# Optimization experiments

Measured on AMD Instinct MI355X. Metric: run time of the kernel, lower is better.

Reference implementation:

```python
import jax, jax.numpy as jnp
import numpy as np

B, CIN, BINS, FRAMES = 8, 2, 1024, 512
NQ = 4
C = 2 * NQ          # number of quantizer channels
E = 1024            # codebook size
BETA = 0.25         # commitment cost


def conv2d(x, w, b, pad):
    y = jax.lax.conv_general_dilated(
        x, w, window_strides=(1, 1),
        padding=((pad[0], pad[0]), (pad[1], pad[1])),
        dimension_numbers=("NCHW", "OIHW", "NCHW"))
    return y + b[None, :, None, None]


def setup_inputs() -> dict:
    key = jax.random.key(0)
    ks = jax.random.split(key, 6)
    return {
        "x": jax.random.normal(ks[0], (B, CIN, BINS, FRAMES), jnp.float32),
        "conv1_w": jax.random.normal(ks[1], (C, CIN, 9, 1), jnp.float32) * 0.1,
        "conv1_b": jnp.zeros((C,), jnp.float32),
        "conv2_w": jax.random.normal(ks[2], (C, C, 9, 1), jnp.float32) * 0.05,
        "conv2_b": jnp.zeros((C,), jnp.float32),
        "skip_w": jax.random.normal(ks[3], (C, CIN, 1, 1), jnp.float32) * 0.1,
        "skip_b": jnp.zeros((C,), jnp.float32),
        "codebooks": jax.random.normal(ks[4], (C, E, BINS), jnp.float32),
    }


def reference(x, conv1_w, conv1_b, conv2_w, conv2_b, skip_w, skip_b, codebooks):
    # ResBlock projection: 2 -> 2*num_quantizers channels, (9,1) convs along bins
    h = conv2d(x, conv1_w, conv1_b, (4, 0))
    h = jax.nn.leaky_relu(h, 0.2)
    h = conv2d(h, conv2_w, conv2_b, (4, 0))
    h = h + conv2d(x, skip_w, skip_b, (0, 0))          # [B, C, BINS, F]

    # Batched VQ across all C quantizers at once.
    # Per-frame vectors: [C, N, BINS] with N = B*FRAMES
    v = jnp.transpose(h, (1, 0, 3, 2)).reshape(C, B * FRAMES, BINS)
    x2 = jnp.sum(v * v, axis=-1, keepdims=True)                     # [C,N,1]
    e2 = jnp.sum(codebooks * codebooks, axis=-1)[:, None, :]        # [C,1,E]
    d = x2 + e2 - 2.0 * jnp.einsum("cnb,ceb->cne", v, codebooks)    # [C,N,E]
    idx = jnp.argmin(d, axis=-1)                                    # [C,N]
    q = jax.vmap(lambda cb, i: cb[i])(codebooks, idx)               # [C,N,BINS]

    # VQ-VAE loss (codebook + commitment), summed over the 2Q quantizers
    sg = jax.lax.stop_gradient
    cb_loss = jnp.mean((q - sg(v)) ** 2, axis=(1, 2))
    cm_loss = jnp.mean((sg(q) - v) ** 2, axis=(1, 2))
    loss = jnp.sum(cb_loss + BETA * cm_loss)

    # straight-through estimator
    q_st = v + sg(q - v)                                            # [C,N,BINS]
    q_st = q_st.reshape(C, B, FRAMES, BINS).transpose(1, 0, 3, 2)   # [B,C,BINS,F]
    # torch loop prepends each new q: final channel order is reversed
    embedded = q_st[:, ::-1]
    return embedded, loss
```

## Files before the change

### kernel.cpp

```cpp
#include <hip/hip_runtime.h>

namespace {

constexpr int kB = 8, kCin = 2, kBins = 1024, kFrames = 512;
constexpr int kC = 8, kE = 1024, kN = kB * kFrames;

typedef _Float16 f16x8 __attribute__((ext_vector_type(8)));
typedef float f32x4 __attribute__((ext_vector_type(4)));

union HPack4 { _Float16 h[4]; uint2 u; };
union HPack2 { _Float16 h[2]; unsigned int u; };

__device__ inline void splitf(float v, _Float16& h, _Float16& l) {
    float a = (fabsf(v) >= 6.103515625e-05f) ? v : 0.f;
    _Float16 hh = (_Float16)a;
    h = hh;
    l = (_Float16)((v - (float)hh) * 4096.0f);
}

constexpr int BT = 32, FT = 32, XB = BT + 16, HB = BT + 8;

__global__ __launch_bounds__(512, 4) void conv_fused_v2d(
    const float* __restrict__ x,
    const float* __restrict__ w1, const float* __restrict__ b1,
    const float* __restrict__ w2, const float* __restrict__ b2,
    const float* __restrict__ wsk, const float* __restrict__ bsk,
    _Float16* __restrict__ V1, float* __restrict__ partials)
{
    __shared__ float xt[kCin][XB][33];
    __shared__ float h1t[kC][HB][33];
    __shared__ float vbuf[2][BT][33];
    __shared__ float w1s[kC * kCin * 9];
    __shared__ float w2s[kC * kC][12];
    __shared__ float wsks[kC * kCin];
    __shared__ float b1s[kC], b2s[kC], bsks[kC];
    __shared__ float reds[8];

    const int t = threadIdx.x;
    const int bt = blockIdx.x, ft = blockIdx.y, bb = blockIdx.z;
    const int bs = bt * BT, f0 = ft * FT;
    _Float16* V2 = V1 + (size_t)33554432;

    if (t < kC * kCin * 9) w1s[t] = w1[t];
    for (int i = t; i < 768; i += 512) {
        int cc = i / 12, k = i % 12;
        w2s[cc][k] = (k < 9) ? w2[cc * 9 + k] : 0.f;
    }
    if (t < kC * kCin) wsks[t] = wsk[t];
    if (t < kC) { b1s[t] = b1[t]; b2s[t] = b2[t]; bsks[t] = bsk[t]; }

    for (int i = t; i < kCin * XB * FT; i += 512) {
        int fi = i % FT, xb = (i / FT) % XB, ci = i / (FT * XB);
        int gb = bs - 8 + xb;
        float v = 0.f;
        if (gb >= 0 && gb < kBins)
            v = x[((bb * kCin + ci) * kBins + gb) * kFrames + f0 + fi];
        xt[ci][xb][fi] = v;
    }
    __syncthreads();

    const int fi = t & 31;
    const int r = t >> 5;
    const int cm = r & 7, rh = r >> 3;

    #pragma unroll
    for (int qi = 0; qi < 3; qi++) {
        const int q = qi * 2 + rh;
        if (q < 5) {
            float a8[8];
            #pragma unroll
            for (int jj = 0; jj < 8; jj++) a8[jj] = b1s[cm];
            #pragma unroll
            for (int ci = 0; ci < kCin; ci++) {
                float w[16];
                #pragma unroll
                for (int k = 0; k < 16; k++) w[k] = xt[ci][q * 8 + k][fi];
                const float* wp = &w1s[(cm * kCin + ci) * 9];
                #pragma unroll
                for (int jj = 0; jj < 8; jj++)
                    #pragma unroll
                    for (int k = 0; k < 9; k++)
                        a8[jj] += w[jj + k] * wp[k];
            }
            #pragma unroll
            for (int jj = 0; jj < 8; jj++) {
                int hb = q * 8 + jj;
                int gb = bs - 4 + hb;
                float v = (gb >= 0 && gb < kBins) ? (a8[jj] > 0.f ? a8[jj] : 0.2f * a8[jj]) : 0.f;
                h1t[cm][hb][fi] = v;
            }
        }
    }
    __syncthreads();

    float acc[8][2];
    #pragma unroll
    for (int c = 0; c < 8; c++)
        #pragma unroll
        for (int j = 0; j < 2; j++) acc[c][j] = b2s[c] + bsks[c];

    for (int ci = 0; ci < 8; ci++) {
        float w[10];
        #pragma unroll
        for (int k = 0; k < 10; k++) w[k] = h1t[ci][r * 2 + k][fi];
        #pragma unroll
        for (int c = 0; c < 8; c++) {
            const float4* wp4 = (const float4*)&w2s[c * 8 + ci][0];
            float4 wA = wp4[0], wB = wp4[1], wC = wp4[2];
            float wk[9] = {wA.x, wA.y, wA.z, wA.w, wB.x, wB.y, wB.z, wB.w, wC.x};
            #pragma unroll
            for (int j = 0; j < 2; j++) {
                float s = 0.f;
                #pragma unroll
                for (int k = 0; k < 9; k++) s += w[j + k] * wk[k];
                acc[c][j] += s;
            }
        }
    }
    #pragma unroll
    for (int j = 0; j < 2; j++) {
        float x0 = xt[0][r * 2 + j + 8][fi];
        float x1 = xt[1][r * 2 + j + 8][fi];
        #pragma unroll
        for (int c = 0; c < 8; c++)
            acc[c][j] += x0 * wsks[c * 2] + x1 * wsks[c * 2 + 1];
    }

    float sq = 0.f;
    #pragma unroll
    for (int c = 0; c < 8; c++)
        #pragma unroll
        for (int j = 0; j < 2; j++) sq += acc[c][j] * acc[c][j];

    const int rn = t >> 4, kq = t & 15;
    #pragma unroll 1
    for (int c = 0; c < 8; c++) {
        vbuf[c & 1][fi][r * 2 + 0] = acc[c][0];
        vbuf[c & 1][fi][r * 2 + 1] = acc[c][1];
        __syncthreads();
        float v0 = vbuf[c & 1][rn][kq * 2 + 0];
        float v1 = vbuf[c & 1][rn][kq * 2 + 1];
        HPack2 ph, pl;
        splitf(v0, ph.h[0], pl.h[0]);
        splitf(v1, ph.h[1], pl.h[1]);
        const int ng = bb * kFrames + f0 + rn;
        const size_t off = ((size_t)(c * kN + ng)) * kBins + bs + kq * 2;
        *(unsigned int*)&V1[off] = ph.u;
        *(unsigned int*)&V2[off] = pl.u;
    }

    #pragma unroll
    for (int off = 32; off > 0; off >>= 1) sq += __shfl_down(sq, off);
    if ((t & 63) == 0) reds[t >> 6] = sq;
    __syncthreads();
    if (t == 0) {
        float s = 0.f;
        #pragma unroll
        for (int i = 0; i < 8; i++) s += reds[i];
        int blin = (bb * gridDim.y + blockIdx.y) * gridDim.x + blockIdx.x;
        partials[blin] = s;
    }
}

__global__ __launch_bounds__(256) void cbsplit_e2(
    const float* __restrict__ cb, _Float16* __restrict__ B1,
    float* __restrict__ e2, unsigned long long* __restrict__ pk)
{
    const int gid = blockIdx.x * 256 + threadIdx.x;
    if (gid < kC * kN) pk[gid] = ~0ull;

    const int gw = gid >> 6;
    const int lane = threadIdx.x & 63;
    _Float16* B2 = B1 + (size_t)8388608;
    const float* row = cb + (size_t)gw * kBins;
    float s = 0.f;
    #pragma unroll
    for (int j = 0; j < 4; j++) {
        float4 v = *(const float4*)&row[lane * 4 + j * 256];
        s += v.x * v.x + v.y * v.y + v.z * v.z + v.w * v.w;
        HPack4 ph, pl;
        splitf(v.x, ph.h[0], pl.h[0]);
        splitf(v.y, ph.h[1], pl.h[1]);
        splitf(v.z, ph.h[2], pl.h[2]);
        splitf(v.w, ph.h[3], pl.h[3]);
        size_t off = (size_t)gw * kBins + lane * 4 + j * 256;
        *(uint2*)&B1[off] = ph.u;
        *(uint2*)&B2[off] = pl.u;
    }
    #pragma unroll
    for (int off = 32; off > 0; off >>= 1) s += __shfl_down(s, off);
    if (lane == 0) e2[gw] = s;
}

__global__ __launch_bounds__(512, 2) void dist_mfma(
    const _Float16* __restrict__ V1, const _Float16* __restrict__ B1p,
    const float* __restrict__ e2, unsigned long long* __restrict__ pk)
{
    __shared__ char smem[3 * 49152 + 2048];

    const int t = threadIdx.x;
    const int bidx = blockIdx.x;
    const int ch = bidx & 7;
    const int eh = (bidx >> 3) & 1;
    const int n0 = (bidx >> 4) * 256;
    const int w = t >> 6, lane = t & 63;
    const int l15 = lane & 15, kc4 = lane >> 4;
    const int wm = w >> 1, we = w & 1;

    float* lds_e2 = (float*)(smem + 147456);
    lds_e2[t] = e2[ch * kE + eh * 512 + t];

    const _Float16* srcA[4];
    int dstA[4];
    #pragma unroll
    for (int i = 0; i < 4; i++) {
        int ci = i * 512 + t;
        int row = ci >> 3, slot = ci & 7;
        int g = slot ^ (row & 7);
        int p = g >> 2, kc = g & 3;
        srcA[i] = V1 + (size_t)p * 33554432 + ((size_t)(ch * kN + n0 + row)) * kBins + kc * 8;
        dstA[i] = ci * 16;
    }
    const _Float16* srcB[2];
    int dstB[2];
    #pragma unroll
    for (int i = 0; i < 2; i++) {
        int bi = i * 512 + t;
        int row = bi >> 3, slot = bi & 7;
        int g = slot ^ (row & 7);
        int p = g >> 2, kc = g & 3;
        srcB[i] = B1p + (size_t)p * 8388608 + ((size_t)(ch * kE + row)) * kBins + kc * 8;
        dstB[i] = 32768 + bi * 16;
    }

    const int rowA = wm * 64 + l15;
    const int rowB = we * 64 + l15;
    const int baseA1 = rowA * 128 + ((kc4) ^ (rowA & 7)) * 16;
    const int baseA2 = rowA * 128 + ((4 + kc4) ^ (rowA & 7)) * 16;
    const int baseB1 = 32768 + rowB * 128 + ((kc4) ^ (rowB & 7)) * 16;
    const int baseB2 = 32768 + rowB * 128 + ((4 + kc4) ^ (rowB & 7)) * 16;

    float rm[16];
    int ri[16];
    #pragma unroll
    for (int s = 0; s < 16; s++) { rm[s] = 3.4e38f; ri[s] = 0; }

    typedef const __attribute__((address_space(1))) void gsrc_t;
    typedef __attribute__((address_space(3))) void gdst_t;

    auto issue = [&](int jj, int bw) {
        const int k0 = (jj & 31) * 32;
        const size_t etoff = (size_t)(eh * 4 + (jj >> 5)) * 128 * kBins + k0;
        char* nb = smem + bw * 49152;
        #pragma unroll
        for (int i = 0; i < 4; i++)
            __builtin_amdgcn_global_load_lds((gsrc_t*)(srcA[i] + k0), (gdst_t*)(nb + dstA[i]), 16, 0, 0);
        #pragma unroll
        for (int i = 0; i < 2; i++)
            __builtin_amdgcn_global_load_lds((gsrc_t*)(srcB[i] + etoff), (gdst_t*)(nb + dstB[i]), 16, 0, 0);
    };

    __syncthreads();

    issue(0, 0);
    issue(1, 1);
    int bread = 0, bwrite = 2;

    #pragma unroll 1
    for (int et = 0; et < 4; et++) {
        f32x4 hi[4][4], lo[4][4];
        #pragma unroll
        for (int mi = 0; mi < 4; mi++)
            #pragma unroll
            for (int ei = 0; ei < 4; ei++) {
                hi[mi][ei] = (f32x4){0.f, 0.f, 0.f, 0.f};
                lo[mi][ei] = (f32x4){0.f, 0.f, 0.f, 0.f};
            }

        #pragma unroll 1
        for (int ks = 0; ks < 32; ks++) {
            const int j = et * 32 + ks;
            if (j < 127)
                asm volatile("s_waitcnt vmcnt(6)\n\ts_barrier" ::: "memory");
            else
                asm volatile("s_waitcnt vmcnt(0)\n\ts_barrier" ::: "memory");
            if (j < 126) {
                issue(j + 2, bwrite);
                bwrite = (bwrite == 2) ? 0 : bwrite + 1;
            }

            const char* buf = smem + bread * 49152;
            bread = (bread == 2) ? 0 : bread + 1;

            f16x8 a1[4], a2[4], b1f[4], b2f[4];
            #pragma unroll
            for (int mi = 0; mi < 4; mi++) {
                a1[mi] = *(const f16x8*)(buf + baseA1 + mi * 2048);
                a2[mi] = *(const f16x8*)(buf + baseA2 + mi * 2048);
            }
            #pragma unroll
            for (int ei = 0; ei < 4; ei++) {
                b1f[ei] = *(const f16x8*)(buf + baseB1 + ei * 2048);
                b2f[ei] = *(const f16x8*)(buf + baseB2 + ei * 2048);
            }
            __builtin_amdgcn_s_setprio(1);
            #pragma unroll
            for (int mi = 0; mi < 4; mi++)
                #pragma unroll
                for (int ei = 0; ei < 4; ei++) {
                    hi[mi][ei] = __builtin_amdgcn_mfma_f32_16x16x32_f16(a1[mi], b1f[ei], hi[mi][ei], 0, 0, 0);
                    lo[mi][ei] = __builtin_amdgcn_mfma_f32_16x16x32_f16(a1[mi], b2f[ei], lo[mi][ei], 0, 0, 0);
                    lo[mi][ei] = __builtin_amdgcn_mfma_f32_16x16x32_f16(a2[mi], b1f[ei], lo[mi][ei], 0, 0, 0);
                }
            __builtin_amdgcn_s_setprio(0);
        }

        #pragma unroll
        for (int ei = 0; ei < 4; ei++) {
            const int eloc = et * 128 + we * 64 + ei * 16 + l15;
            const float ev = lds_e2[eloc];
            const int eix = eh * 512 + eloc;
            #pragma unroll
            for (int mi = 0; mi < 4; mi++) {
                f32x4 dot4 = hi[mi][ei] + lo[mi][ei] * (1.0f / 4096.0f);
                #pragma unroll
                for (int rr = 0; rr < 4; rr++) {
                    float d = ev - 2.0f * dot4[rr];
                    int s = mi * 4 + rr;
                    if (d < rm[s]) { rm[s] = d; ri[s] = eix; }
                }
            }
        }
    }

    #pragma unroll
    for (int m = 1; m < 16; m <<= 1) {
        #pragma unroll
        for (int s = 0; s < 16; s++) {
            float ov = __shfl_xor(rm[s], m);
            int oi = __shfl_xor(ri[s], m);
            if (ov < rm[s] || (ov == rm[s] && oi < ri[s])) { rm[s] = ov; ri[s] = oi; }
        }
    }

    float* mv = (float*)smem;
    int* miv = (int*)(smem + 2048);
    __syncthreads();
    if (l15 == 0) {
        #pragma unroll
        for (int s = 0; s < 16; s++) {
            int mi = s >> 2, rr = s & 3;
            int rloc = wm * 64 + mi * 16 + (lane >> 4) * 4 + rr;
            mv[rloc * 2 + we] = rm[s];
            miv[rloc * 2 + we] = ri[s];
        }
    }
    __syncthreads();
    if (t < 256) {
        float v0 = mv[t * 2], v1 = mv[t * 2 + 1];
        int i0 = miv[t * 2], i1 = miv[t * 2 + 1];
        bool take1 = (v1 < v0) || (v1 == v0 && i1 < i0);
        float bv = take1 ? v1 : v0;
        int bi = take1 ? i1 : i0;
        unsigned int u = __float_as_uint(bv);
        unsigned int su = (u & 0x80000000u) ? ~u : (u ^ 0x80000000u);
        unsigned long long packed = ((unsigned long long)su << 32) | (unsigned int)bi;
        atomicMin(&pk[ch * kN + n0 + t], packed);
    }
}

__global__ __launch_bounds__(256) void gather_pk(
    const float* __restrict__ cb, const unsigned long long* __restrict__ pk,
    const float* __restrict__ partials, float* __restrict__ out,
    float* __restrict__ loss)
{
    const int t = threadIdx.x;
    const int lane = t & 63, q = t >> 6;
    const int b = blockIdx.x;
    const int cp = b & 7;
    const int bt = (b >> 3) & 63;
    const int ftile = (b >> 9) & 7;
    const int bb = b >> 12;
    const int co = (kC - 1) - cp;
    const int f = ftile * 64 + lane;
    const int n = bb * kFrames + f;
    const int e = (int)(unsigned int)(pk[cp * kN + n] & 0xFFFFFFFFull);
    const int bin0 = bt * 16 + q * 4;
    const float4 v4 = *(const float4*)&cb[((size_t)cp * kE + e) * kBins + bin0];
    const size_t base = ((size_t)(bb * kC + co) * kBins + bin0) * kFrames + f;
    out[base] = v4.x;
    out[base + kFrames] = v4.y;
    out[base + 2 * (size_t)kFrames] = v4.z;
    out[base + 3 * (size_t)kFrames] = v4.w;

    if (b == 32767) {
        __shared__ float reds[256];
        float s = 0.f;
        for (int i = t; i < kC * kN; i += 256) {
            unsigned int su = (unsigned int)(pk[i] >> 32);
            unsigned int u = (su & 0x80000000u) ? (su ^ 0x80000000u) : ~su;
            s += __uint_as_float(u);
        }
        for (int i = t; i < 4096; i += 256) s += partials[i];
        reds[t] = s;
        __syncthreads();
        for (int off = 128; off > 0; off >>= 1) {
            if (t < off) reds[t] += reds[t + off];
            __syncthreads();
        }
        if (t == 0) loss[0] = 1.25f * reds[0] / (float)(kN * kBins);
    }
}

}

extern "C" void kernel_launch(void* const* d_in, const int* in_sizes, int n_in,
                              void* d_out, int out_size, void* d_ws, size_t ws_size,
                              hipStream_t stream)
{
    const float* x   = (const float*)d_in[0];
    const float* w1  = (const float*)d_in[1];
    const float* b1  = (const float*)d_in[2];
    const float* w2  = (const float*)d_in[3];
    const float* b2  = (const float*)d_in[4];
    const float* wsk = (const float*)d_in[5];
    const float* bsk = (const float*)d_in[6];
    const float* cb  = (const float*)d_in[7];
    float* out = (float*)d_out;
    char* ws = (char*)d_ws;

    _Float16* B1 = (_Float16*)ws;
    float* e2                  = (float*)(ws + 33554432);
    unsigned long long* pk     = (unsigned long long*)(ws + 33554432 + 32768);
    float* partials            = (float*)(ws + 33554432 + 32768 + 262144);
    _Float16* V1 = (_Float16*)d_out;

    conv_fused_v2d<<<dim3(kBins / BT, kFrames / FT, kB), 512, 0, stream>>>(
        x, w1, b1, w2, b2, wsk, bsk, V1, partials);
    cbsplit_e2<<<(kC * kE) / 4, 256, 0, stream>>>(cb, B1, e2, pk);
    dist_mfma<<<dim3(256), 512, 0, stream>>>(V1, B1, e2, pk);
    gather_pk<<<dim3(32768), 256, 0, stream>>>(cb, pk, partials, out,
                                               out + (size_t)kC * kBins * kN);
}
```

Baseline: 390.1 us.

## Switch distance MFMA to 32x32x16 tiles and reduce argmin via LDS atomics

The distance kernel now uses 32x32x16 f16 MFMA instructions instead of 16x16x32, with a 2x2 tile of 32x32 accumulators per wave covering the same 64x64 output and the same hi/lo split-precision scheme. The per-thread running argmin, shuffle reduction and staging arrays are replaced by packed 64-bit atomicMin operations into an LDS array after each codebook tile. Larger MFMA tiles reduce LDS fragment reads per FLOP and may raise MFMA throughput. The per-element LDS atomics, 64 per thread per tile, add contention and instruction overhead in the epilogue.

```diff
diff --git a/kernel.cpp b/kernel.cpp
--- a/kernel.cpp
+++ b/kernel.cpp
@@ -6,7 +6,7 @@
 constexpr int kC = 8, kE = 1024, kN = kB * kFrames;
 
 typedef _Float16 f16x8 __attribute__((ext_vector_type(8)));
-typedef float f32x4 __attribute__((ext_vector_type(4)));
+typedef float f32x16 __attribute__((ext_vector_type(16)));
 
 union HPack4 { _Float16 h[4]; uint2 u; };
 union HPack2 { _Float16 h[2]; unsigned int u; };
@@ -196,7 +196,7 @@
     const _Float16* __restrict__ V1, const _Float16* __restrict__ B1p,
     const float* __restrict__ e2, unsigned long long* __restrict__ pk)
 {
-    __shared__ char smem[3 * 49152 + 2048];
+    __shared__ char smem[3 * 49152 + 2048 + 4096];
 
     const int t = threadIdx.x;
     const int bidx = blockIdx.x;
@@ -204,11 +204,13 @@
     const int eh = (bidx >> 3) & 1;
     const int n0 = (bidx >> 4) * 256;
     const int w = t >> 6, lane = t & 63;
-    const int l15 = lane & 15, kc4 = lane >> 4;
+    const int l31 = lane & 31, h = lane >> 5;
     const int wm = w >> 1, we = w & 1;
 
     float* lds_e2 = (float*)(smem + 147456);
+    unsigned long long* pkLds = (unsigned long long*)(smem + 149504);
     lds_e2[t] = e2[ch * kE + eh * 512 + t];
+    pkLds[t] = ~0ull;
 
     const _Float16* srcA[4];
     int dstA[4];
@@ -233,17 +235,15 @@
         dstB[i] = 32768 + bi * 16;
     }
 
-    const int rowA = wm * 64 + l15;
-    const int rowB = we * 64 + l15;
-    const int baseA1 = rowA * 128 + ((kc4) ^ (rowA & 7)) * 16;
-    const int baseA2 = rowA * 128 + ((4 + kc4) ^ (rowA & 7)) * 16;
-    const int baseB1 = 32768 + rowB * 128 + ((kc4) ^ (rowB & 7)) * 16;
-    const int baseB2 = 32768 + rowB * 128 + ((4 + kc4) ^ (rowB & 7)) * 16;
-
-    float rm[16];
-    int ri[16];
-    #pragma unroll
-    for (int s = 0; s < 16; s++) { rm[s] = 3.4e38f; ri[s] = 0; }
+    const int rowA0 = (wm * 64 + l31) * 128;
+    const int rowB0 = 32768 + (we * 64 + l31) * 128;
+    int offP0[2], offP1[2];
+    #pragma unroll
+    for (int ks2 = 0; ks2 < 2; ks2++) {
+        int kc = ks2 * 2 + h;
+        offP0[ks2] = ((kc) ^ (l31 & 7)) * 16;
+        offP1[ks2] = ((4 + kc) ^ (l31 & 7)) * 16;
+    }
 
     typedef const __attribute__((address_space(1))) void gsrc_t;
     typedef __attribute__((address_space(3))) void gdst_t;
@@ -268,13 +268,13 @@
 
     #pragma unroll 1
     for (int et = 0; et < 4; et++) {
-        f32x4 hi[4][4], lo[4][4];
-        #pragma unroll
-        for (int mi = 0; mi < 4; mi++)
-            #pragma unroll
-            for (int ei = 0; ei < 4; ei++) {
-                hi[mi][ei] = (f32x4){0.f, 0.f, 0.f, 0.f};
-                lo[mi][ei] = (f32x4){0.f, 0.f, 0.f, 0.f};
+        f32x16 hi[2][2], lo[2][2];
+        #pragma unroll
+        for (int mi = 0; mi < 2; mi++)
+            #pragma unroll
+            for (int ei = 0; ei < 2; ei++) {
+                hi[mi][ei] = (f32x16)(0.f);
+                lo[mi][ei] = (f32x16)(0.f);
             }
 
         #pragma unroll 1
@@ -292,80 +292,62 @@
             const char* buf = smem + bread * 49152;
             bread = (bread == 2) ? 0 : bread + 1;
 
-            f16x8 a1[4], a2[4], b1f[4], b2f[4];
-            #pragma unroll
-            for (int mi = 0; mi < 4; mi++) {
-                a1[mi] = *(const f16x8*)(buf + baseA1 + mi * 2048);
-                a2[mi] = *(const f16x8*)(buf + baseA2 + mi * 2048);
-            }
-            #pragma unroll
-            for (int ei = 0; ei < 4; ei++) {
-                b1f[ei] = *(const f16x8*)(buf + baseB1 + ei * 2048);
-                b2f[ei] = *(const f16x8*)(buf + baseB2 + ei * 2048);
-            }
+            f16x8 a1[2][2], a2[2][2], b1f[2][2], b2f[2][2];
+            #pragma unroll
+            for (int mi = 0; mi < 2; mi++)
+                #pragma unroll
+                for (int ks2 = 0; ks2 < 2; ks2++) {
+                    a1[mi][ks2] = *(const f16x8*)(buf + rowA0 + mi * 4096 + offP0[ks2]);
+                    a2[mi][ks2] = *(const f16x8*)(buf + rowA0 + mi * 4096 + offP1[ks2]);
+                }
+            #pragma unroll
+            for (int ei = 0; ei < 2; ei++)
+                #pragma unroll
+                for (int ks2 = 0; ks2 < 2; ks2++) {
+                    b1f[ei][ks2] = *(const f16x8*)(buf + rowB0 + ei * 4096 + offP0[ks2]);
+                    b2f[ei][ks2] = *(const f16x8*)(buf + rowB0 + ei * 4096 + offP1[ks2]);
+                }
             __builtin_amdgcn_s_setprio(1);
             #pragma unroll
-            for (int mi = 0; mi < 4; mi++)
-                #pragma unroll
-                for (int ei = 0; ei < 4; ei++) {
-                    hi[mi][ei] = __builtin_amdgcn_mfma_f32_16x16x32_f16(a1[mi], b1f[ei], hi[mi][ei], 0, 0, 0);
-                    lo[mi][ei] = __builtin_amdgcn_mfma_f32_16x16x32_f16(a1[mi], b2f[ei], lo[mi][ei], 0, 0, 0);
-                    lo[mi][ei] = __builtin_amdgcn_mfma_f32_16x16x32_f16(a2[mi], b1f[ei], lo[mi][ei], 0, 0, 0);
+            for (int ks2 = 0; ks2 < 2; ks2++)
+                #pragma unroll
+                for (int mi = 0; mi < 2; mi++)
+                    #pragma unroll
+                    for (int ei = 0; ei < 2; ei++) {
+                        hi[mi][ei] = __builtin_amdgcn_mfma_f32_32x32x16_f16(a1[mi][ks2], b1f[ei][ks2], hi[mi][ei], 0, 0, 0);
+                        lo[mi][ei] = __builtin_amdgcn_mfma_f32_32x32x16_f16(a1[mi][ks2], b2f[ei][ks2], lo[mi][ei], 0, 0, 0);
+                        lo[mi][ei] = __builtin_amdgcn_mfma_f32_32x32x16_f16(a2[mi][ks2], b1f[ei][ks2], lo[mi][ei], 0, 0, 0);
+                    }
+            __builtin_amdgcn_s_setprio(0);
+        }
+
+        #pragma unroll
+        for (int ei = 0; ei < 2; ei++) {
+            const int ecol = we * 64 + ei * 32 + l31;
+            const float ev = lds_e2[et * 128 + ecol];
+            const int eix = eh * 512 + et * 128 + ecol;
+            #pragma unroll
+            for (int mi = 0; mi < 2; mi++) {
+                #pragma unroll
+                for (int reg = 0; reg < 16; reg++) {
+                    float dot = hi[mi][ei][reg] + lo[mi][ei][reg] * (1.0f / 4096.0f);
+                    float d = ev - 2.0f * dot;
+                    int rloc = wm * 64 + mi * 32 + (reg & 3) + 8 * (reg >> 2) + 4 * h;
+                    unsigned int u = __float_as_uint(d);
+                    unsigned int su = (u & 0x80000000u) ? ~u : (u ^ 0x80000000u);
+                    unsigned long long packed =
+                        ((unsigned long long)su << 32) | (unsigned int)eix;
+                    atomicMin(&pkLds[rloc * 2 + we], packed);
                 }
-            __builtin_amdgcn_s_setprio(0);
-        }
-
-        #pragma unroll
-        for (int ei = 0; ei < 4; ei++) {
-            const int eloc = et * 128 + we * 64 + ei * 16 + l15;
-            const float ev = lds_e2[eloc];
-            const int eix = eh * 512 + eloc;
-            #pragma unroll
-            for (int mi = 0; mi < 4; mi++) {
-                f32x4 dot4 = hi[mi][ei] + lo[mi][ei] * (1.0f / 4096.0f);
-                #pragma unroll
-                for (int rr = 0; rr < 4; rr++) {
-                    float d = ev - 2.0f * dot4[rr];
-                    int s = mi * 4 + rr;
-                    if (d < rm[s]) { rm[s] = d; ri[s] = eix; }
-                }
-            }
-        }
-    }
-
-    #pragma unroll
-    for (int m = 1; m < 16; m <<= 1) {
-        #pragma unroll
-        for (int s = 0; s < 16; s++) {
-            float ov = __shfl_xor(rm[s], m);
-            int oi = __shfl_xor(ri[s], m);
-            if (ov < rm[s] || (ov == rm[s] && oi < ri[s])) { rm[s] = ov; ri[s] = oi; }
-        }
-    }
-
-    float* mv = (float*)smem;
-    int* miv = (int*)(smem + 2048);
-    __syncthreads();
-    if (l15 == 0) {
-        #pragma unroll
-        for (int s = 0; s < 16; s++) {
-            int mi = s >> 2, rr = s & 3;
-            int rloc = wm * 64 + mi * 16 + (lane >> 4) * 4 + rr;
-            mv[rloc * 2 + we] = rm[s];
-            miv[rloc * 2 + we] = ri[s];
-        }
-    }
+            }
+        }
+    }
+
     __syncthreads();
     if (t < 256) {
-        float v0 = mv[t * 2], v1 = mv[t * 2 + 1];
-        int i0 = miv[t * 2], i1 = miv[t * 2 + 1];
-        bool take1 = (v1 < v0) || (v1 == v0 && i1 < i0);
-        float bv = take1 ? v1 : v0;
-        int bi = take1 ? i1 : i0;
-        unsigned int u = __float_as_uint(bv);
-        unsigned int su = (u & 0x80000000u) ? ~u : (u ^ 0x80000000u);
-        unsigned long long packed = ((unsigned long long)su << 32) | (unsigned int)bi;
-        atomicMin(&pk[ch * kN + n0 + t], packed);
+        unsigned long long p0 = pkLds[t * 2], p1 = pkLds[t * 2 + 1];
+        unsigned long long pmin = (p1 < p0) ? p1 : p0;
+        atomicMin(&pk[ch * kN + n0 + t], pmin);
     }
 }
 
```

New measurement: 509.9 us. +30.7%, slower.
